# Kernel tuning notes

Measured on AMD Instinct MI355X. Metric: run time of the kernel, lower is better.

The kernel has to match this reference:

```python
import jax, jax.numpy as jnp
import numpy as np

B, N, M, E2, NE, NF = 64, 512, 30, 4, 32, 64
NE4 = NE // 4  # 8


def setup_inputs() -> dict:
    key = jax.random.key(0)
    ks = jax.random.split(key, 20)
    s = 0.1
    inp = {
        'Sg': jax.random.uniform(ks[0], (B, N, M, E2), dtype=jnp.float32),
        'R': jax.random.normal(ks[1], (B, N, M, 4), dtype=jnp.float32),
        # mlp_emb: Linear(E2,NE) -> Sigmoid -> Linear(NE,NE) -> Tanh -> Linear(NE,NE)
        'We0': jax.random.normal(ks[2], (E2, NE), dtype=jnp.float32) * s,
        'be0': jnp.zeros((NE,), jnp.float32),
        'We1': jax.random.normal(ks[3], (NE, NE), dtype=jnp.float32) * s,
        'be1': jnp.zeros((NE,), jnp.float32),
        'We2': jax.random.normal(ks[4], (NE, NE), dtype=jnp.float32) * s,
        'be2': jnp.zeros((NE,), jnp.float32),
        # mlp_fit: Linear(256,NF)->Tanh->Linear(NF,NF)->Sigmoid->Linear(NF,NF)->Tanh->Linear(NF,1)
        'Wf0': jax.random.normal(ks[5], (NE * NE4, NF), dtype=jnp.float32) * s,
        'bf0': jnp.zeros((NF,), jnp.float32),
        'Wf1': jax.random.normal(ks[6], (NF, NF), dtype=jnp.float32) * s,
        'bf1': jnp.zeros((NF,), jnp.float32),
        'Wf2': jax.random.normal(ks[7], (NF, NF), dtype=jnp.float32) * s,
        'bf2': jnp.zeros((NF,), jnp.float32),
        'Wf3': jax.random.normal(ks[8], (NF, 1), dtype=jnp.float32) * s,
        'bf3': jnp.zeros((1,), jnp.float32),
    }
    return inp


def reference(Sg, R, We0, be0, We1, be1, We2, be2,
              Wf0, bf0, Wf1, bf1, Wf2, bf2, Wf3, bf3):
    # Per-pair embedding MLP G: [B,N,M,E2] -> [B,N,M,NE]
    h = jax.nn.sigmoid(Sg @ We0 + be0)
    h = jnp.tanh(h @ We1 + be1)
    G = h @ We2 + be2  # [B,N,M,NE]

    # Dmat = einsum('uijk,uijl,uiml,uimn->uikn', G[...,:NE4], R, R, G)
    # Fused as two batched GEMMs to avoid the 4-operand contraction.
    A = jnp.einsum('uijk,uijl->uikl', G[..., :NE4], R)   # [B,N,NE4,4]
    Bm = jnp.einsum('uiml,uimn->uiln', R, G)             # [B,N,4,NE]
    D = jnp.einsum('uikl,uiln->uikn', A, Bm)             # [B,N,NE4,NE]
    D = D.reshape(D.shape[0], D.shape[1], NE4 * NE)      # [B,N,256]

    # fit MLP -> [B,N,1]
    h = jnp.tanh(D @ Wf0 + bf0)
    h = jax.nn.sigmoid(h @ Wf1 + bf1)
    h = jnp.tanh(h @ Wf2 + bf2)
    Q = h @ Wf3 + bf3                                    # [B,N,1]
    return jnp.mean(Q, axis=(1, 2))                      # [B]
```

## Files before the change

kernel.cpp:

```cpp
#include <hip/hip_runtime.h>

#define BB 64
#define NN 512
#define MM 30
#define E2 4
#define NE 32
#define NE4 8
#define NF 64
#define BN_TOTAL (BB * NN)
#define TP 36
#define HP 65

typedef __attribute__((ext_vector_type(8))) short bf16x8;
typedef __attribute__((ext_vector_type(4))) float vf4;

__device__ __forceinline__ float frcp(float x) { return __builtin_amdgcn_rcpf(x); }
__device__ __forceinline__ float fsig(float x)  { return frcp(1.0f + __expf(-x)); }
__device__ __forceinline__ float ftanh(float x) { return 1.0f - 2.0f * frcp(1.0f + __expf(2.0f * x)); }

union fragu { unsigned u[4]; bf16x8 v; };

__device__ __forceinline__ unsigned cvt_pk_bf16(float a, float b) {
    unsigned r;
    asm("v_cvt_pk_bf16_f32 %0, %1, %2" : "=v"(r) : "v"(a), "v"(b));
    return r;
}
__device__ __forceinline__ float lo16f(unsigned u) { return __uint_as_float(u << 16); }
__device__ __forceinline__ float hi16f(unsigned u) { return __uint_as_float(u & 0xFFFF0000u); }

__device__ __forceinline__ void split8v(vf4 a, vf4 b, bf16x8& hi, bf16x8& lo) {
    fragu H, L;
    H.u[0] = cvt_pk_bf16(a.x, a.y);
    H.u[1] = cvt_pk_bf16(a.z, a.w);
    H.u[2] = cvt_pk_bf16(b.x, b.y);
    H.u[3] = cvt_pk_bf16(b.z, b.w);
    L.u[0] = cvt_pk_bf16(a.x - lo16f(H.u[0]), a.y - hi16f(H.u[0]));
    L.u[1] = cvt_pk_bf16(a.z - lo16f(H.u[1]), a.w - hi16f(H.u[1]));
    L.u[2] = cvt_pk_bf16(b.x - lo16f(H.u[2]), b.y - hi16f(H.u[2]));
    L.u[3] = cvt_pk_bf16(b.z - lo16f(H.u[3]), b.w - hi16f(H.u[3]));
    hi = H.v; lo = L.v;
}

__device__ __forceinline__ vf4 mm3(bf16x8 ah, bf16x8 al, bf16x8 bh, bf16x8 bl, vf4 c) {
    c = __builtin_amdgcn_mfma_f32_16x16x32_bf16(ah, bh, c, 0, 0, 0);
    c = __builtin_amdgcn_mfma_f32_16x16x32_bf16(ah, bl, c, 0, 0, 0);
    c = __builtin_amdgcn_mfma_f32_16x16x32_bf16(al, bh, c, 0, 0, 0);
    return c;
}

__device__ __forceinline__ vf4 ld4(const float* p) { return *(const vf4*)p; }

__global__ __launch_bounds__(256) void k_prep(
    const float* __restrict__ We1, const float* __restrict__ We2,
    const float* __restrict__ Wf0,
    bf16x8* __restrict__ fragsE, bf16x8* __restrict__ fragsF)
{
    const int tid  = threadIdx.x;
    const int l    = tid & 63;
    const int row0 = l & 15;
    const int grp  = l >> 4;

    if (blockIdx.x < 8) {
        const int combo = blockIdx.x * 4 + (tid >> 6);
        const int k  = combo >> 2;
        const int nt = combo & 3;
        const float* wp = Wf0 + (size_t)(k * 32 + grp * 8) * NF + nt * 16 + row0;
        vf4 x0 = { wp[0],      wp[NF],     wp[2 * NF], wp[3 * NF] };
        vf4 x1 = { wp[4 * NF], wp[5 * NF], wp[6 * NF], wp[7 * NF] };
        bf16x8 h, lo;
        split8v(x0, x1, h, lo);
        fragsF[(combo * 2 + 0) * 64 + l] = h;
        fragsF[(combo * 2 + 1) * 64 + l] = lo;
    } else if (tid < 64) {
#pragma unroll
        for (int nt = 0; nt < 2; ++nt) {
            const float* wp = We1 + (size_t)(grp * 8) * NE + nt * 16 + row0;
            vf4 x0 = { wp[0],      wp[NE],     wp[2 * NE], wp[3 * NE] };
            vf4 x1 = { wp[4 * NE], wp[5 * NE], wp[6 * NE], wp[7 * NE] };
            bf16x8 h, lo;
            split8v(x0, x1, h, lo);
            fragsE[(0 + nt) * 64 + l] = h;
            fragsE[(2 + nt) * 64 + l] = lo;
            const float* wq = We2 + (size_t)(grp * 8) * NE + nt * 16 + row0;
            vf4 y0 = { wq[0],      wq[NE],     wq[2 * NE], wq[3 * NE] };
            vf4 y1 = { wq[4 * NE], wq[5 * NE], wq[6 * NE], wq[7 * NE] };
            split8v(y0, y1, h, lo);
            fragsE[(4 + nt) * 64 + l] = h;
            fragsE[(6 + nt) * 64 + l] = lo;
        }
    }
}

__global__ __launch_bounds__(256) void k_emb_mfma(
    const float* __restrict__ Sg, const float* __restrict__ R,
    const float* __restrict__ We0, const float* __restrict__ be0,
    const float* __restrict__ be1, const float* __restrict__ be2,
    const bf16x8* __restrict__ frags,
    float* __restrict__ Dout)
{
    __shared__ float T[4][32 * TP];
    __shared__ vf4   Rl[4][32];

    const int tid  = threadIdx.x;
    const int w    = tid >> 6;
    const int l    = tid & 63;
    const int row0 = l & 15;
    const int grp  = l >> 4;
    const int pair = blockIdx.x * 4 + w;

    if (l < 32) {
        vf4 rv = 0.f;
        if (l < MM) rv = ld4(R + ((size_t)pair * MM + l) * 4);
        Rl[w][l] = rv;
    }

    bf16x8 B1h[2], B1l[2], B2h[2], B2l[2];
#pragma unroll
    for (int nt = 0; nt < 2; ++nt) {
        B1h[nt] = frags[(0 + nt) * 64 + l];
        B1l[nt] = frags[(2 + nt) * 64 + l];
        B2h[nt] = frags[(4 + nt) * 64 + l];
        B2l[nt] = frags[(6 + nt) * 64 + l];
    }

    vf4 w0[4][2];
#pragma unroll
    for (int i = 0; i < 4; ++i) {
        w0[i][0] = ld4(We0 + i * NE + grp * 8);
        w0[i][1] = ld4(We0 + i * NE + grp * 8 + 4);
    }
    const vf4 b0a = ld4(be0 + grp * 8);
    const vf4 b0b = ld4(be0 + grp * 8 + 4);
    const float bias1[2] = { be1[row0], be1[row0 + 16] };
    const float bias2[2] = { be2[row0], be2[row0 + 16] };

    bf16x8 Ah[2], Al[2];
#pragma unroll
    for (int t = 0; t < 2; ++t) {
        const int p = 16 * t + row0;
        vf4 s = 0.f;
        if (p < MM) s = ld4(Sg + ((size_t)pair * MM + p) * 4);
        vf4 acc0 = b0a + s.x * w0[0][0] + s.y * w0[1][0] + s.z * w0[2][0] + s.w * w0[3][0];
        vf4 acc1 = b0b + s.x * w0[0][1] + s.y * w0[1][1] + s.z * w0[2][1] + s.w * w0[3][1];
#pragma unroll
        for (int e = 0; e < 4; ++e) { acc0[e] = fsig(acc0[e]); acc1[e] = fsig(acc1[e]); }
        split8v(acc0, acc1, Ah[t], Al[t]);
    }

    vf4 H1[2][2];
#pragma unroll
    for (int t = 0; t < 2; ++t)
#pragma unroll
        for (int nt = 0; nt < 2; ++nt) {
            vf4 c = bias1[nt];
            H1[t][nt] = mm3(Ah[t], Al[t], B1h[nt], B1l[nt], c);
        }

#pragma unroll
    for (int t = 0; t < 2; ++t)
#pragma unroll
        for (int nt = 0; nt < 2; ++nt)
#pragma unroll
            for (int e = 0; e < 4; ++e)
                T[w][(grp * 4 + e + 16 * t) * TP + row0 + 16 * nt] = ftanh(H1[t][nt][e]);

    bf16x8 A2h[2], A2l[2];
#pragma unroll
    for (int t = 0; t < 2; ++t) {
        const float* src = &T[w][(16 * t + row0) * TP + grp * 8];
        vf4 x0 = *(const vf4*)(src);
        vf4 x1 = *(const vf4*)(src + 4);
        split8v(x0, x1, A2h[t], A2l[t]);
    }

    vf4 G[2][2];
#pragma unroll
    for (int t = 0; t < 2; ++t)
#pragma unroll
        for (int nt = 0; nt < 2; ++nt) {
            vf4 c = bias2[nt];
            G[t][nt] = mm3(A2h[t], A2l[t], B2h[nt], B2l[nt], c);
        }

    float bm[4][2] = {{0.f, 0.f}, {0.f, 0.f}, {0.f, 0.f}, {0.f, 0.f}};
#pragma unroll
    for (int t = 0; t < 2; ++t)
#pragma unroll
        for (int e = 0; e < 4; ++e) {
            const int rrow = grp * 4 + e + 16 * t;
            const vf4 r4 = Rl[w][rrow];
#pragma unroll
            for (int nt = 0; nt < 2; ++nt) {
                const float gv = G[t][nt][e];
                bm[0][nt] += r4.x * gv;
                bm[1][nt] += r4.y * gv;
                bm[2][nt] += r4.z * gv;
                bm[3][nt] += r4.w * gv;
            }
        }
    float bmv[4][2];
#pragma unroll
    for (int li = 0; li < 4; ++li)
#pragma unroll
        for (int nt = 0; nt < 2; ++nt) {
            float v = bm[li][nt];
            v += __shfl_xor(v, 16);
            v += __shfl_xor(v, 32);
            bmv[li][nt] = v;
        }

    float d[2][2] = {{0.f, 0.f}, {0.f, 0.f}};
#pragma unroll
    for (int kk = 0; kk < 2; ++kk) {
        const int src = grp * 2 + kk;
#pragma unroll
        for (int li = 0; li < 4; ++li) {
            const float a = __shfl(bmv[li][0], src);
#pragma unroll
            for (int nt = 0; nt < 2; ++nt) d[kk][nt] += a * bmv[li][nt];
        }
    }

    float* __restrict__ dp = Dout + (size_t)pair * 256;
#pragma unroll
    for (int kk = 0; kk < 2; ++kk)
#pragma unroll
        for (int nt = 0; nt < 2; ++nt)
            dp[(grp * 2 + kk) * NE + nt * 16 + row0] = d[kk][nt];
}

__global__ __launch_bounds__(256) void k_fit3(
    const float* __restrict__ D, const bf16x8* __restrict__ fragsF,
    const float* __restrict__ bf0,
    const float* __restrict__ Wf1, const float* __restrict__ bf1,
    const float* __restrict__ Wf2, const float* __restrict__ bf2,
    const float* __restrict__ Wf3, const float* __restrict__ bf3,
    float* __restrict__ Q)
{
    __shared__ float HT0[64 * HP];
    __shared__ float HT1[64 * 64];

    const int tid  = threadIdx.x;
    const int wv   = tid >> 6;
    const int l    = tid & 63;
    const int row0 = l & 15;
    const int grp  = l >> 4;
    const int r    = l;

    {
        const float* __restrict__ drow =
            D + (size_t)(blockIdx.x * 64 + wv * 16 + row0) * 256;

        vf4 c[4];
#pragma unroll
        for (int nt = 0; nt < 4; ++nt) c[nt] = bf0[nt * 16 + row0];

#pragma unroll
        for (int k = 0; k < 8; ++k) {
            vf4 x0 = ld4(drow + k * 32 + grp * 8);
            vf4 x1 = ld4(drow + k * 32 + grp * 8 + 4);
            bf16x8 ah, al;
            split8v(x0, x1, ah, al);
#pragma unroll
            for (int nt = 0; nt < 4; ++nt) {
                const int combo = k * 4 + nt;
                const bf16x8 bh = fragsF[(combo * 2 + 0) * 64 + l];
                const bf16x8 bl = fragsF[(combo * 2 + 1) * 64 + l];
                c[nt] = mm3(ah, al, bh, bl, c[nt]);
            }
        }

#pragma unroll
        for (int nt = 0; nt < 4; ++nt)
#pragma unroll
            for (int e = 0; e < 4; ++e)
                HT0[(nt * 16 + row0) * HP + wv * 16 + grp * 4 + e] = ftanh(c[nt][e]);
    }
    __syncthreads();

    const int f0 = __builtin_amdgcn_readfirstlane(wv) * 16;

    float h2[16];
#pragma unroll
    for (int j = 0; j < 16; ++j) h2[j] = bf1[f0 + j];
#pragma unroll 8
    for (int k = 0; k < 64; ++k) {
        const float hv = HT0[k * HP + r];
        const float* __restrict__ wv1 = Wf1 + (size_t)k * NF + f0;
#pragma unroll
        for (int j = 0; j < 16; ++j) h2[j] += hv * wv1[j];
    }
#pragma unroll
    for (int j = 0; j < 16; ++j) HT1[(f0 + j) * 64 + r] = fsig(h2[j]);
    __syncthreads();

    float h[16];
#pragma unroll
    for (int j = 0; j < 16; ++j) h[j] = bf2[f0 + j];
#pragma unroll 8
    for (int k = 0; k < 64; ++k) {
        const float hv = HT1[k * 64 + r];
        const float* __restrict__ wv2 = Wf2 + (size_t)k * NF + f0;
#pragma unroll
        for (int j = 0; j < 16; ++j) h[j] += hv * wv2[j];
    }

    float qp = 0.f;
#pragma unroll
    for (int j = 0; j < 16; ++j) qp += ftanh(h[j]) * Wf3[f0 + j];

    float* Qp = HT1;
    __syncthreads();
    Qp[wv * 64 + r] = qp;
    __syncthreads();

    if (tid < 64) {
        const float q = bf3[0] + Qp[tid] + Qp[64 + tid] + Qp[128 + tid] + Qp[192 + tid];
        Q[(size_t)blockIdx.x * 64 + tid] = q;
    }
}

__global__ __launch_bounds__(256) void k_mean(const float* __restrict__ Q,
                                              float* __restrict__ out)
{
    __shared__ float s[256];
    const int b = blockIdx.x;
    const int t = threadIdx.x;
    float v = Q[b * NN + t] + Q[b * NN + 256 + t];
    s[t] = v;
    __syncthreads();
#pragma unroll
    for (int off = 128; off > 0; off >>= 1) {
        if (t < off) s[t] += s[t + off];
        __syncthreads();
    }
    if (t == 0) out[b] = s[0] * (1.0f / (float)NN);
}

extern "C" void kernel_launch(void* const* d_in, const int* in_sizes, int n_in,
                              void* d_out, int out_size, void* d_ws, size_t ws_size,
                              hipStream_t stream)
{
    const float* Sg  = (const float*)d_in[0];
    const float* R   = (const float*)d_in[1];
    const float* We0 = (const float*)d_in[2];
    const float* be0 = (const float*)d_in[3];
    const float* We1 = (const float*)d_in[4];
    const float* be1 = (const float*)d_in[5];
    const float* We2 = (const float*)d_in[6];
    const float* be2 = (const float*)d_in[7];
    const float* Wf0 = (const float*)d_in[8];
    const float* bf0 = (const float*)d_in[9];
    const float* Wf1 = (const float*)d_in[10];
    const float* bf1 = (const float*)d_in[11];
    const float* Wf2 = (const float*)d_in[12];
    const float* bf2 = (const float*)d_in[13];
    const float* Wf3 = (const float*)d_in[14];
    const float* bf3 = (const float*)d_in[15];

    char* ws = (char*)d_ws;
    float*  Dm     = (float*)ws;
    float*  Q      = (float*)(ws + (size_t)BN_TOTAL * 256 * 4);
    bf16x8* fragsE = (bf16x8*)(ws + (size_t)BN_TOTAL * 256 * 4
                                  + (size_t)BN_TOTAL * 4);
    bf16x8* fragsF = (bf16x8*)(ws + (size_t)BN_TOTAL * 256 * 4
                                  + (size_t)BN_TOTAL * 4 + 8192);

    k_prep<<<9, 256, 0, stream>>>(We1, We2, Wf0, fragsE, fragsF);
    k_emb_mfma<<<BN_TOTAL / 4, 256, 0, stream>>>(Sg, R, We0, be0, be1, be2, fragsE, Dm);
    k_fit3<<<BN_TOTAL / 64, 256, 0, stream>>>(Dm, fragsF, bf0, Wf1, bf1, Wf2, bf2, Wf3, bf3, Q);
    k_mean<<<BB, 256, 0, stream>>>(Q, (float*)d_out);
}
```

Before: 71.32 us.

## Run fit MLP layers 1 and 2 on MFMA with split-bf16 weight fragments

Layers 1 and 2 of the fit MLP were scalar FMA loops over shared memory with per-thread weight loads. They now run as bf16 MFMA GEMMs using a three-term hi/lo split, with Wf1/Wf2 fragments prepared by extra blocks in k_prep. Each wave now owns its 16 rows end to end, so two block-wide syncs are removed and the final projection is reduced with shuffles. The cost is extra split conversions and the extra prep blocks, and precision now depends on the bf16x3 emulation.

```diff
diff --git a/kernel.cpp b/kernel.cpp
--- a/kernel.cpp
+++ b/kernel.cpp
@@ -52,16 +52,19 @@
 
 __global__ __launch_bounds__(256) void k_prep(
     const float* __restrict__ We1, const float* __restrict__ We2,
-    const float* __restrict__ Wf0,
-    bf16x8* __restrict__ fragsE, bf16x8* __restrict__ fragsF)
+    const float* __restrict__ Wf0, const float* __restrict__ Wf1,
+    const float* __restrict__ Wf2,
+    bf16x8* __restrict__ fragsE, bf16x8* __restrict__ fragsF,
+    bf16x8* __restrict__ fragsG1, bf16x8* __restrict__ fragsG2)
 {
     const int tid  = threadIdx.x;
     const int l    = tid & 63;
     const int row0 = l & 15;
     const int grp  = l >> 4;
-
-    if (blockIdx.x < 8) {
-        const int combo = blockIdx.x * 4 + (tid >> 6);
+    const int bid  = blockIdx.x;
+
+    if (bid < 8) {
+        const int combo = bid * 4 + (tid >> 6);
         const int k  = combo >> 2;
         const int nt = combo & 3;
         const float* wp = Wf0 + (size_t)(k * 32 + grp * 8) * NF + nt * 16 + row0;
@@ -71,6 +74,20 @@
         split8v(x0, x1, h, lo);
         fragsF[(combo * 2 + 0) * 64 + l] = h;
         fragsF[(combo * 2 + 1) * 64 + l] = lo;
+    } else if (bid < 12) {
+        const int layer = (bid - 8) >> 1;
+        const int combo = ((bid - 8) & 1) * 4 + (tid >> 6);
+        const int ktile = combo >> 2;
+        const int nt    = combo & 3;
+        const float* W  = layer ? Wf2 : Wf1;
+        bf16x8* out     = layer ? fragsG2 : fragsG1;
+        const float* wp = W + (size_t)(ktile * 32 + grp * 8) * NF + nt * 16 + row0;
+        vf4 x0 = { wp[0],      wp[NF],     wp[2 * NF], wp[3 * NF] };
+        vf4 x1 = { wp[4 * NF], wp[5 * NF], wp[6 * NF], wp[7 * NF] };
+        bf16x8 h, lo;
+        split8v(x0, x1, h, lo);
+        out[(combo * 2 + 0) * 64 + l] = h;
+        out[(combo * 2 + 1) * 64 + l] = lo;
     } else if (tid < 64) {
 #pragma unroll
         for (int nt = 0; nt < 2; ++nt) {
@@ -229,23 +246,23 @@
             dp[(grp * 2 + kk) * NE + nt * 16 + row0] = d[kk][nt];
 }
 
-__global__ __launch_bounds__(256) void k_fit3(
+__global__ __launch_bounds__(256) void k_fit4(
     const float* __restrict__ D, const bf16x8* __restrict__ fragsF,
-    const float* __restrict__ bf0,
-    const float* __restrict__ Wf1, const float* __restrict__ bf1,
-    const float* __restrict__ Wf2, const float* __restrict__ bf2,
+    const bf16x8* __restrict__ fragsG1, const bf16x8* __restrict__ fragsG2,
+    const float* __restrict__ bf0, const float* __restrict__ bf1,
+    const float* __restrict__ bf2,
     const float* __restrict__ Wf3, const float* __restrict__ bf3,
     float* __restrict__ Q)
 {
     __shared__ float HT0[64 * HP];
-    __shared__ float HT1[64 * 64];
+    __shared__ float HT1[64 * HP];
+    __shared__ float Qp[64];
 
     const int tid  = threadIdx.x;
     const int wv   = tid >> 6;
     const int l    = tid & 63;
     const int row0 = l & 15;
     const int grp  = l >> 4;
-    const int r    = l;
 
     {
         const float* __restrict__ drow =
@@ -264,60 +281,90 @@
 #pragma unroll
             for (int nt = 0; nt < 4; ++nt) {
                 const int combo = k * 4 + nt;
-                const bf16x8 bh = fragsF[(combo * 2 + 0) * 64 + l];
-                const bf16x8 bl = fragsF[(combo * 2 + 1) * 64 + l];
-                c[nt] = mm3(ah, al, bh, bl, c[nt]);
-            }
-        }
-
+                c[nt] = mm3(ah, al, fragsF[(combo * 2 + 0) * 64 + l],
+                                    fragsF[(combo * 2 + 1) * 64 + l], c[nt]);
+            }
+        }
 #pragma unroll
         for (int nt = 0; nt < 4; ++nt)
 #pragma unroll
             for (int e = 0; e < 4; ++e)
                 HT0[(nt * 16 + row0) * HP + wv * 16 + grp * 4 + e] = ftanh(c[nt][e]);
     }
+
+    {
+        vf4 c[4];
+#pragma unroll
+        for (int nt = 0; nt < 4; ++nt) c[nt] = bf1[nt * 16 + row0];
+#pragma unroll
+        for (int ktile = 0; ktile < 2; ++ktile) {
+            vf4 x0, x1;
+#pragma unroll
+            for (int e = 0; e < 4; ++e) {
+                x0[e] = HT0[(ktile * 32 + grp * 8 + e) * HP + wv * 16 + row0];
+                x1[e] = HT0[(ktile * 32 + grp * 8 + 4 + e) * HP + wv * 16 + row0];
+            }
+            bf16x8 ah, al;
+            split8v(x0, x1, ah, al);
+#pragma unroll
+            for (int nt = 0; nt < 4; ++nt) {
+                const int combo = ktile * 4 + nt;
+                c[nt] = mm3(ah, al, fragsG1[(combo * 2 + 0) * 64 + l],
+                                    fragsG1[(combo * 2 + 1) * 64 + l], c[nt]);
+            }
+        }
+#pragma unroll
+        for (int nt = 0; nt < 4; ++nt)
+#pragma unroll
+            for (int e = 0; e < 4; ++e)
+                HT1[(nt * 16 + row0) * HP + wv * 16 + grp * 4 + e] = fsig(c[nt][e]);
+    }
+
+    vf4 c2[4];
+    {
+#pragma unroll
+        for (int nt = 0; nt < 4; ++nt) c2[nt] = bf2[nt * 16 + row0];
+#pragma unroll
+        for (int ktile = 0; ktile < 2; ++ktile) {
+            vf4 x0, x1;
+#pragma unroll
+            for (int e = 0; e < 4; ++e) {
+                x0[e] = HT1[(ktile * 32 + grp * 8 + e) * HP + wv * 16 + row0];
+                x1[e] = HT1[(ktile * 32 + grp * 8 + 4 + e) * HP + wv * 16 + row0];
+            }
+            bf16x8 ah, al;
+            split8v(x0, x1, ah, al);
+#pragma unroll
+            for (int nt = 0; nt < 4; ++nt) {
+                const int combo = ktile * 4 + nt;
+                c2[nt] = mm3(ah, al, fragsG2[(combo * 2 + 0) * 64 + l],
+                                     fragsG2[(combo * 2 + 1) * 64 + l], c2[nt]);
+            }
+        }
+    }
+
+    {
+        float p[4] = {0.f, 0.f, 0.f, 0.f};
+#pragma unroll
+        for (int nt = 0; nt < 4; ++nt) {
+            const float w3 = Wf3[nt * 16 + row0];
+#pragma unroll
+            for (int e = 0; e < 4; ++e) p[e] += ftanh(c2[nt][e]) * w3;
+        }
+#pragma unroll
+        for (int e = 0; e < 4; ++e) {
+            float v = p[e];
+            v += __shfl_xor(v, 1);
+            v += __shfl_xor(v, 2);
+            v += __shfl_xor(v, 4);
+            v += __shfl_xor(v, 8);
+            if (row0 == 0) Qp[wv * 16 + grp * 4 + e] = v;
+        }
+    }
     __syncthreads();
 
-    const int f0 = __builtin_amdgcn_readfirstlane(wv) * 16;
-
-    float h2[16];
-#pragma unroll
-    for (int j = 0; j < 16; ++j) h2[j] = bf1[f0 + j];
-#pragma unroll 8
-    for (int k = 0; k < 64; ++k) {
-        const float hv = HT0[k * HP + r];
-        const float* __restrict__ wv1 = Wf1 + (size_t)k * NF + f0;
-#pragma unroll
-        for (int j = 0; j < 16; ++j) h2[j] += hv * wv1[j];
-    }
-#pragma unroll
-    for (int j = 0; j < 16; ++j) HT1[(f0 + j) * 64 + r] = fsig(h2[j]);
-    __syncthreads();
-
-    float h[16];
-#pragma unroll
-    for (int j = 0; j < 16; ++j) h[j] = bf2[f0 + j];
-#pragma unroll 8
-    for (int k = 0; k < 64; ++k) {
-        const float hv = HT1[k * 64 + r];
-        const float* __restrict__ wv2 = Wf2 + (size_t)k * NF + f0;
-#pragma unroll
-        for (int j = 0; j < 16; ++j) h[j] += hv * wv2[j];
-    }
-
-    float qp = 0.f;
-#pragma unroll
-    for (int j = 0; j < 16; ++j) qp += ftanh(h[j]) * Wf3[f0 + j];
-
-    float* Qp = HT1;
-    __syncthreads();
-    Qp[wv * 64 + r] = qp;
-    __syncthreads();
-
-    if (tid < 64) {
-        const float q = bf3[0] + Qp[tid] + Qp[64 + tid] + Qp[128 + tid] + Qp[192 + tid];
-        Q[(size_t)blockIdx.x * 64 + tid] = q;
-    }
+    if (tid < 64)
+        Q[(size_t)blockIdx.x * 64 + tid] = bf3[0] + Qp[tid];
 }
 
 __global__ __launch_bounds__(256) void k_mean(const float* __restrict__ Q,
@@ -359,15 +406,18 @@
     const float* bf3 = (const float*)d_in[15];
 
     char* ws = (char*)d_ws;
-    float*  Dm     = (float*)ws;
-    float*  Q      = (float*)(ws + (size_t)BN_TOTAL * 256 * 4);
-    bf16x8* fragsE = (bf16x8*)(ws + (size_t)BN_TOTAL * 256 * 4
-                                  + (size_t)BN_TOTAL * 4);
-    bf16x8* fragsF = (bf16x8*)(ws + (size_t)BN_TOTAL * 256 * 4
-                                  + (size_t)BN_TOTAL * 4 + 8192);
-
-    k_prep<<<9, 256, 0, stream>>>(We1, We2, Wf0, fragsE, fragsF);
+    float*  Dm      = (float*)ws;
+    float*  Q       = (float*)(ws + (size_t)BN_TOTAL * 256 * 4);
+    char*   tb      = ws + (size_t)BN_TOTAL * 256 * 4 + (size_t)BN_TOTAL * 4;
+    bf16x8* fragsE  = (bf16x8*)tb;
+    bf16x8* fragsF  = (bf16x8*)(tb + 8192);
+    bf16x8* fragsG1 = (bf16x8*)(tb + 8192 + 65536);
+    bf16x8* fragsG2 = (bf16x8*)(tb + 8192 + 65536 + 16384);
+
+    k_prep<<<13, 256, 0, stream>>>(We1, We2, Wf0, Wf1, Wf2,
+                                   fragsE, fragsF, fragsG1, fragsG2);
     k_emb_mfma<<<BN_TOTAL / 4, 256, 0, stream>>>(Sg, R, We0, be0, be1, be2, fragsE, Dm);
-    k_fit3<<<BN_TOTAL / 64, 256, 0, stream>>>(Dm, fragsF, bf0, Wf1, bf1, Wf2, bf2, Wf3, bf3, Q);
+    k_fit4<<<BN_TOTAL / 64, 256, 0, stream>>>(Dm, fragsF, fragsG1, fragsG2,
+                                              bf0, bf1, bf2, Wf3, bf3, Q);
     k_mean<<<BB, 256, 0, stream>>>(Q, (float*)d_out);
 }
```

Measured after the change: 68.60 us. 1.04x faster.
